# Performance work log

Hardware: AMD Instinct MI355X
Metric: run time of the kernel (lower is better)

## Reference

```python
import jax, jax.numpy as jnp
import numpy as np

DIM = 4096
NUM_HEAD = 32
NUM_KV_HEAD = 8
ROPE_THETA = 10000.0
B, T = 2, 2048


def apply_rope(x, start_pos=0, theta=ROPE_THETA):
    # x: [B, T, H, d_head]; rotate half-split pairs by position-dependent angles
    d = x.shape[-1]
    half = d // 2
    inv_freq = 1.0 / (theta ** (jnp.arange(0, half, dtype=jnp.float32) / half))
    pos = jnp.arange(x.shape[1], dtype=jnp.float32) + start_pos  # [T]
    ang = pos[:, None] * inv_freq[None, :]                       # [T, half]
    cos = jnp.cos(ang)[None, :, None, :]
    sin = jnp.sin(ang)[None, :, None, :]
    x1, x2 = x[..., :half], x[..., half:]
    return jnp.concatenate([x1 * cos - x2 * sin, x1 * sin + x2 * cos], axis=-1)


def setup_inputs() -> dict:
    key = jax.random.key(0)
    ks = jax.random.split(key, 5)
    scale = 0.02
    X = jax.random.normal(ks[0], (B, T, DIM), dtype=jnp.float32)
    Wq = jax.random.normal(ks[1], (DIM, DIM), dtype=jnp.float32) * scale
    Wk = jax.random.normal(ks[2], (DIM, DIM // NUM_HEAD * NUM_KV_HEAD), dtype=jnp.float32) * scale
    Wv = jax.random.normal(ks[3], (DIM, DIM // NUM_HEAD * NUM_KV_HEAD), dtype=jnp.float32) * scale
    Wo = jax.random.normal(ks[4], (DIM, DIM), dtype=jnp.float32) * scale
    return {"X": X, "Wq": Wq, "Wk": Wk, "Wv": Wv, "Wo": Wo}


def reference(X, Wq, Wk, Wv, Wo):
    Bs, Ts, C = X.shape
    H, Hkv = NUM_HEAD, NUM_KV_HEAD
    dh = C // H
    G = H // Hkv  # GQA group size

    Q = apply_rope((X @ Wq).reshape(Bs, Ts, H, dh))      # [B,T,H,dh]
    K = apply_rope((X @ Wk).reshape(Bs, Ts, Hkv, dh))    # [B,T,Hkv,dh]
    V = (X @ Wv).reshape(Bs, Ts, Hkv, dh)                # [B,T,Hkv,dh]

    # [B,Hkv,G,T,dh]: grouped layout equivalent to repeat_interleave on head dim
    Qh = Q.transpose(0, 2, 1, 3).reshape(Bs, Hkv, G, Ts, dh)
    Kh = K.transpose(0, 2, 1, 3)  # [B,Hkv,T,dh]
    Vh = V.transpose(0, 2, 1, 3)

    scores = jnp.einsum('bkgtd,bksd->bkgts', Qh, Kh) / jnp.sqrt(jnp.float32(dh))
    causal = jnp.tril(jnp.ones((Ts, Ts), dtype=bool))
    scores = jnp.where(causal[None, None, None], scores, -jnp.inf)
    attn = jax.nn.softmax(scores, axis=-1)
    out = jnp.einsum('bkgts,bksd->bkgtd', attn, Vh)       # [B,Hkv,G,T,dh]
    out = out.reshape(Bs, H, Ts, dh).transpose(0, 2, 1, 3).reshape(Bs, Ts, C)
    return out @ Wo
```

## Files before the change

### kernel.cpp

```cpp
#include <hip/hip_runtime.h>
#include <hip/hip_bf16.h>
#include <cstdint>
#include <cstddef>

#define B_   2
#define T_   2048
#define DIM_ 4096
#define H_   32
#define HKV_ 8
#define DH_  128
#define MROWS (B_*T_)

typedef __bf16 bf16_t;
typedef bf16_t bf16x8 __attribute__((ext_vector_type(8)));
typedef bf16_t bf16x4 __attribute__((ext_vector_type(4)));
typedef float  f32x4  __attribute__((ext_vector_type(4)));

typedef __attribute__((address_space(1))) void gvoid_t;
typedef __attribute__((address_space(3))) void lvoid_t;

__device__ __forceinline__ void gld_lds16(const void* g, void* l) {
  __builtin_amdgcn_global_load_lds((gvoid_t*)g, (lvoid_t*)l, 16, 0, 0);
}

__device__ __forceinline__ f32x4 mfma16(bf16x8 a, bf16x8 b, f32x4 c) {
  return __builtin_amdgcn_mfma_f32_16x16x32_bf16(a, b, c, 0, 0, 0);
}

__global__ void cast_f32_bf16(const float* __restrict__ in,
                              bf16_t* __restrict__ out, int n4) {
  int i = blockIdx.x * blockDim.x + threadIdx.x;
  if (i < n4) {
    float4 v = ((const float4*)in)[i];
    bf16x4 o;
    o[0] = (bf16_t)v.x; o[1] = (bf16_t)v.y; o[2] = (bf16_t)v.z; o[3] = (bf16_t)v.w;
    ((bf16x4*)out)[i] = o;
  }
}

__global__ void transpose_cast(const float* __restrict__ in,
                               bf16_t* __restrict__ out, int K, int N) {
  __shared__ float tile[32][33];
  int n0 = blockIdx.x * 32, k0 = blockIdx.y * 32;
  int tx = threadIdx.x, ty = threadIdx.y;
#pragma unroll
  for (int j = 0; j < 4; ++j)
    tile[ty + j*8][tx] = in[(size_t)(k0 + ty + j*8) * N + n0 + tx];
  __syncthreads();
#pragma unroll
  for (int j = 0; j < 4; ++j)
    out[(size_t)(n0 + ty + j*8) * K + k0 + tx] = (bf16_t)tile[tx][ty + j*8];
}

template <int OUT_F32>
__global__ __launch_bounds__(256, 2)
void gemm_bt(const bf16_t* __restrict__ A, const bf16_t* __restrict__ BT,
             void* __restrict__ C, int M, int N, int K) {
  __shared__ __align__(16) bf16_t Als[128 * 32];
  __shared__ __align__(16) bf16_t Bls[128 * 32];
  const int tid  = threadIdx.x;
  const int wave = tid >> 6, lane = tid & 63;
  const int quad = lane >> 4, l16 = lane & 15;
  const int wm = wave >> 1, wn = wave & 1;
  const int m0 = blockIdx.y * 128, n0 = blockIdx.x * 128;

  f32x4 acc[4][4] = {};

  const int srow = lane >> 2;
  const int scol = (lane & 3) * 8;

  for (int k0 = 0; k0 < K; k0 += 32) {
#pragma unroll
    for (int c = 0; c < 2; ++c) {
      int ch = wave * 2 + c;
      gld_lds16(A + (size_t)(m0 + ch*16 + srow) * K + k0 + scol,
                &Als[ch*512 + srow*32 + scol]);
    }
#pragma unroll
    for (int c = 0; c < 2; ++c) {
      int ch = wave * 2 + c;
      gld_lds16(BT + (size_t)(n0 + ch*16 + srow) * K + k0 + scol,
                &Bls[ch*512 + srow*32 + scol]);
    }
    __syncthreads();

    bf16x8 af[4], bfr[4];
#pragma unroll
    for (int mi = 0; mi < 4; ++mi)
      af[mi] = *(const bf16x8*)&Als[(wm*64 + mi*16 + l16)*32 + quad*8];
#pragma unroll
    for (int ni = 0; ni < 4; ++ni)
      bfr[ni] = *(const bf16x8*)&Bls[(wn*64 + ni*16 + l16)*32 + quad*8];
#pragma unroll
    for (int mi = 0; mi < 4; ++mi)
#pragma unroll
      for (int ni = 0; ni < 4; ++ni)
        acc[mi][ni] = mfma16(af[mi], bfr[ni], acc[mi][ni]);
    __syncthreads();
  }

#pragma unroll
  for (int mi = 0; mi < 4; ++mi)
#pragma unroll
    for (int ni = 0; ni < 4; ++ni)
#pragma unroll
      for (int r = 0; r < 4; ++r) {
        int row = m0 + wm*64 + mi*16 + quad*4 + r;
        int col = n0 + wn*64 + ni*16 + l16;
        if (OUT_F32)
          ((float*)C)[(size_t)row * N + col] = acc[mi][ni][r];
        else
          ((bf16_t*)C)[(size_t)row * N + col] = (bf16_t)acc[mi][ni][r];
      }
}

__global__ void rope_kernel(bf16_t* __restrict__ X, int Hn, int total) {
  int i = blockIdx.x * blockDim.x + threadIdx.x;
  if (i >= total) return;
  int d   = i & 63;
  int rem = i >> 6;
  int h   = rem % Hn; rem /= Hn;
  int t   = rem % T_;
  int b   = rem / T_;
  size_t base = ((size_t)(b * T_ + t) * Hn + h) * DH_;
  float x1 = (float)X[base + d];
  float x2 = (float)X[base + 64 + d];
  float inv_freq = expf(-(float)d * 0.14391156758f);
  float ang = (float)t * inv_freq;
  float s, c;
  sincosf(ang, &s, &c);
  X[base + d]      = (bf16_t)(x1 * c - x2 * s);
  X[base + 64 + d] = (bf16_t)(x1 * s + x2 * c);
}

__global__ void v_transpose(const bf16_t* __restrict__ Vb,
                            bf16_t* __restrict__ VT) {
  __shared__ bf16_t tile[32][33];
  int t0 = blockIdx.x * 32;
  int d0 = blockIdx.y * 32;
  int bk = blockIdx.z;
  int b = bk >> 3, kv = bk & 7;
  int tx = threadIdx.x, ty = threadIdx.y;
#pragma unroll
  for (int j = 0; j < 4; ++j)
    tile[ty + j*8][tx] =
        Vb[(size_t)(b * T_ + t0 + ty + j*8) * (HKV_*DH_) + kv*DH_ + d0 + tx];
  __syncthreads();
#pragma unroll
  for (int j = 0; j < 4; ++j)
    VT[((size_t)bk * DH_ + d0 + ty + j*8) * T_ + t0 + tx] = tile[tx][ty + j*8];
}

__global__ __launch_bounds__(256, 2)
void flash_attn(const bf16_t* __restrict__ Qb, const bf16_t* __restrict__ Kb,
                const bf16_t* __restrict__ VT, bf16_t* __restrict__ Ob) {
  __shared__ __align__(16) bf16_t Kls[64 * 128];
  __shared__ __align__(16) bf16_t Vls[128 * 64];
  __shared__ __align__(16) bf16_t Pls[128 * 72];

  const int tid = threadIdx.x, wave = tid >> 6, lane = tid & 63;
  const int quad = lane >> 4, l16 = lane & 15;
  const int qt = blockIdx.x, h = blockIdx.y, b = blockIdx.z;
  const int kv = h >> 2;

  bf16x8 q[2][4];
#pragma unroll
  for (int mi = 0; mi < 2; ++mi) {
    const bf16_t* base =
        Qb + (size_t)(b*T_ + qt*128 + wave*32 + mi*16 + l16) * DIM_ + h*DH_;
#pragma unroll
    for (int kk = 0; kk < 4; ++kk)
      q[mi][kk] = *(const bf16x8*)(base + kk*32 + quad*8);
  }

  float m_st[2][4], l_st[2][4];
  f32x4 o_acc[2][8] = {};
#pragma unroll
  for (int mi = 0; mi < 2; ++mi)
#pragma unroll
    for (int r = 0; r < 4; ++r) { m_st[mi][r] = -3e38f; l_st[mi][r] = 0.f; }

  const int nkv = 2 * (qt + 1);
  for (int kvt = 0; kvt < nkv; ++kvt) {
    __syncthreads();

    {
      int r_in = lane >> 4, cphys = lane & 15;
#pragma unroll
      for (int c = 0; c < 4; ++c) {
        int ch = wave * 4 + c;
        int krow = ch * 4 + r_in;
        int clog = cphys ^ (krow & 7);
        gld_lds16(Kb + (size_t)(b*T_ + kvt*64 + krow) * (HKV_*DH_) + kv*DH_ + clog*8,
                  &Kls[ch*512 + lane*8]);
      }
      int r8 = lane >> 3, c8 = lane & 7;
#pragma unroll
      for (int c = 0; c < 4; ++c) {
        int ch = wave * 4 + c;
        int drow = ch * 8 + r8;
        int clog = c8 ^ (drow & 7);
        gld_lds16(VT + ((size_t)(b*HKV_ + kv) * DH_ + drow) * T_ + kvt*64 + clog*8,
                  &Vls[ch*512 + lane*8]);
      }
    }
    __syncthreads();

    f32x4 s[2][4] = {};
#pragma unroll
    for (int kk = 0; kk < 4; ++kk) {
      bf16x8 kf[4];
#pragma unroll
      for (int ni = 0; ni < 4; ++ni) {
        int krow = ni*16 + l16;
        int cphys = (kk*4 + quad) ^ (krow & 7);
        kf[ni] = *(const bf16x8*)&Kls[krow*128 + cphys*8];
      }
#pragma unroll
      for (int mi = 0; mi < 2; ++mi)
#pragma unroll
        for (int ni = 0; ni < 4; ++ni)
          s[mi][ni] = mfma16(q[mi][kk], kf[ni], s[mi][ni]);
    }

    const float sc = 0.08838834764831845f;
    const bool need_mask = (kvt >= 2*qt);
#pragma unroll
    for (int mi = 0; mi < 2; ++mi) {
      float al[4];
#pragma unroll
      for (int r = 0; r < 4; ++r) {
        int rpos = qt*128 + wave*32 + mi*16 + quad*4 + r;
        float mx = -3e38f;
#pragma unroll
        for (int ni = 0; ni < 4; ++ni) {
          float v = s[mi][ni][r] * sc;
          if (need_mask) {
            int cpos = kvt*64 + ni*16 + l16;
            if (cpos > rpos) v = -3e38f;
          }
          s[mi][ni][r] = v;
          mx = fmaxf(mx, v);
        }
#pragma unroll
        for (int off = 1; off < 16; off <<= 1)
          mx = fmaxf(mx, __shfl_xor(mx, off, 64));
        float mnew = fmaxf(m_st[mi][r], mx);
        float alpha = __expf(m_st[mi][r] - mnew);
        m_st[mi][r] = mnew;
        float rs = 0.f;
#pragma unroll
        for (int ni = 0; ni < 4; ++ni) {
          float p = __expf(s[mi][ni][r] - mnew);
          s[mi][ni][r] = p;
          rs += p;
        }
#pragma unroll
        for (int off = 1; off < 16; off <<= 1)
          rs += __shfl_xor(rs, off, 64);
        l_st[mi][r] = l_st[mi][r] * alpha + rs;
        al[r] = alpha;
      }
#pragma unroll
      for (int ni = 0; ni < 8; ++ni)
#pragma unroll
        for (int r = 0; r < 4; ++r) o_acc[mi][ni][r] *= al[r];
#pragma unroll
      for (int ni = 0; ni < 4; ++ni)
#pragma unroll
        for (int r = 0; r < 4; ++r) {
          int prow = wave*32 + mi*16 + quad*4 + r;
          Pls[prow*72 + ni*16 + l16] = (bf16_t)s[mi][ni][r];
        }
    }
    __syncthreads();

#pragma unroll
    for (int kk = 0; kk < 2; ++kk) {
      bf16x8 pf[2], vf[8];
#pragma unroll
      for (int mi = 0; mi < 2; ++mi) {
        int prow = wave*32 + mi*16 + l16;
        pf[mi] = *(const bf16x8*)&Pls[prow*72 + kk*32 + quad*8];
      }
#pragma unroll
      for (int ni = 0; ni < 8; ++ni) {
        int drow = ni*16 + l16;
        int cphys = (kk*4 + quad) ^ (drow & 7);
        vf[ni] = *(const bf16x8*)&Vls[drow*64 + cphys*8];
      }
#pragma unroll
      for (int mi = 0; mi < 2; ++mi)
#pragma unroll
        for (int ni = 0; ni < 8; ++ni)
          o_acc[mi][ni] = mfma16(pf[mi], vf[ni], o_acc[mi][ni]);
    }
  }

#pragma unroll
  for (int mi = 0; mi < 2; ++mi) {
    float inv[4];
#pragma unroll
    for (int r = 0; r < 4; ++r) inv[r] = 1.f / l_st[mi][r];
#pragma unroll
    for (int ni = 0; ni < 8; ++ni)
#pragma unroll
      for (int r = 0; r < 4; ++r) {
        size_t row = (size_t)(b*T_ + qt*128 + wave*32 + mi*16 + quad*4 + r);
        int col = h*DH_ + ni*16 + l16;
        Ob[row * DIM_ + col] = (bf16_t)(o_acc[mi][ni][r] * inv[r]);
      }
  }
}

extern "C" void kernel_launch(void* const* d_in, const int* in_sizes, int n_in,
                              void* d_out, int out_size, void* d_ws, size_t ws_size,
                              hipStream_t stream) {
  const float* X  = (const float*)d_in[0];
  const float* Wq = (const float*)d_in[1];
  const float* Wk = (const float*)d_in[2];
  const float* Wv = (const float*)d_in[3];
  const float* Wo = (const float*)d_in[4];
  float* out = (float*)d_out;

  char* ws = (char*)d_ws;
  const size_t SZ_X  = (size_t)MROWS * DIM_ * 2;
  const size_t SZ_WQ = (size_t)DIM_ * DIM_ * 2;
  const size_t SZ_WK = (size_t)DIM_ * 1024 * 2;
  bf16_t* Xb  = (bf16_t*)(ws);
  bf16_t* WqT = (bf16_t*)(ws + SZ_X);
  bf16_t* WkT = (bf16_t*)(ws + SZ_X + SZ_WQ);
  bf16_t* WvT = (bf16_t*)(ws + SZ_X + SZ_WQ + SZ_WK);
  bf16_t* WoT = (bf16_t*)(ws + SZ_X + SZ_WQ + 2*SZ_WK);
  bf16_t* Qb  = (bf16_t*)(ws + SZ_X + 2*SZ_WQ + 2*SZ_WK);
  bf16_t* Kb  = (bf16_t*)(ws + 2*SZ_X + 2*SZ_WQ + 2*SZ_WK);
  bf16_t* Vb  = (bf16_t*)(ws + 2*SZ_X + 2*SZ_WQ + 3*SZ_WK);
  bf16_t* VT  = (bf16_t*)(ws + 2*SZ_X + 2*SZ_WQ + 4*SZ_WK);
  bf16_t* Ob  = Xb;

  {
    int n4 = MROWS * DIM_ / 4;
    cast_f32_bf16<<<(n4 + 255)/256, 256, 0, stream>>>(X, Xb, n4);
  }
  transpose_cast<<<dim3(DIM_/32, DIM_/32), dim3(32,8), 0, stream>>>(Wq, WqT, DIM_, DIM_);
  transpose_cast<<<dim3(1024/32, DIM_/32), dim3(32,8), 0, stream>>>(Wk, WkT, DIM_, 1024);
  transpose_cast<<<dim3(1024/32, DIM_/32), dim3(32,8), 0, stream>>>(Wv, WvT, DIM_, 1024);
  transpose_cast<<<dim3(DIM_/32, DIM_/32), dim3(32,8), 0, stream>>>(Wo, WoT, DIM_, DIM_);

  gemm_bt<0><<<dim3(DIM_/128, MROWS/128), 256, 0, stream>>>(Xb, WqT, Qb, MROWS, DIM_, DIM_);
  gemm_bt<0><<<dim3(1024/128, MROWS/128), 256, 0, stream>>>(Xb, WkT, Kb, MROWS, 1024, DIM_);
  gemm_bt<0><<<dim3(1024/128, MROWS/128), 256, 0, stream>>>(Xb, WvT, Vb, MROWS, 1024, DIM_);

  {
    int totq = B_ * T_ * H_ * 64;
    rope_kernel<<<(totq + 255)/256, 256, 0, stream>>>(Qb, H_, totq);
    int totk = B_ * T_ * HKV_ * 64;
    rope_kernel<<<(totk + 255)/256, 256, 0, stream>>>(Kb, HKV_, totk);
  }

  v_transpose<<<dim3(T_/32, DH_/32, B_*HKV_), dim3(32,8), 0, stream>>>(Vb, VT);

  flash_attn<<<dim3(T_/128, H_, B_), 256, 0, stream>>>(Qb, Kb, VT, Ob);

  gemm_bt<1><<<dim3(DIM_/128, MROWS/128), 256, 0, stream>>>(Ob, WoT, out, MROWS, DIM_, DIM_);
}
```

Baseline: 995.5 us.

## Double-buffer K/V tiles, reverse tile order, and defer softmax rescaling in flash attention

K and V tiles now alternate between two LDS buffers, so the next tile's global-to-LDS copy is issued while the current tile is computed. This removes one barrier per iteration, and the barrier after the P write is dropped because each wave reads only its own P rows. Query tiles run in reverse order so the longest causal blocks start first, and the softmax scale is folded into exp2 arguments. Output rescaling is skipped while the running max stays within a threshold. The P buffer switches from padding to an XOR swizzle, and s_setprio raises wave priority around the MFMA sections. These changes add complexity and LDS usage, and deferred rescaling relies on the threshold keeping exponentials in range.

```diff
diff --git a/kernel.cpp b/kernel.cpp
--- a/kernel.cpp
+++ b/kernel.cpp
@@ -154,13 +154,14 @@
 __global__ __launch_bounds__(256, 2)
 void flash_attn(const bf16_t* __restrict__ Qb, const bf16_t* __restrict__ Kb,
                 const bf16_t* __restrict__ VT, bf16_t* __restrict__ Ob) {
-  __shared__ __align__(16) bf16_t Kls[64 * 128];
-  __shared__ __align__(16) bf16_t Vls[128 * 64];
-  __shared__ __align__(16) bf16_t Pls[128 * 72];
+  __shared__ __align__(16) bf16_t Kls[2][64 * 128];
+  __shared__ __align__(16) bf16_t Vls[2][128 * 64];
+  __shared__ __align__(16) bf16_t Pls[128 * 64];
 
   const int tid = threadIdx.x, wave = tid >> 6, lane = tid & 63;
   const int quad = lane >> 4, l16 = lane & 15;
-  const int qt = blockIdx.x, h = blockIdx.y, b = blockIdx.z;
+  const int qt = (int)gridDim.x - 1 - (int)blockIdx.x;
+  const int h = blockIdx.y, b = blockIdx.z;
   const int kv = h >> 2;
 
   bf16x8 q[2][4];
@@ -178,35 +179,43 @@
 #pragma unroll
   for (int mi = 0; mi < 2; ++mi)
 #pragma unroll
-    for (int r = 0; r < 4; ++r) { m_st[mi][r] = -3e38f; l_st[mi][r] = 0.f; }
+    for (int r = 0; r < 4; ++r) { m_st[mi][r] = -1e30f; l_st[mi][r] = 0.f; }
 
   const int nkv = 2 * (qt + 1);
+
+  auto stage = [&](int kvt, int pb) {
+    int r_in = lane >> 4, cph = lane & 15;
+#pragma unroll
+    for (int c = 0; c < 4; ++c) {
+      int ch = wave * 4 + c;
+      int krow = ch * 4 + r_in;
+      int clog = cph ^ (krow & 7);
+      gld_lds16(Kb + (size_t)(b*T_ + kvt*64 + krow) * (HKV_*DH_) + kv*DH_ + clog*8,
+                &Kls[pb][ch*512 + lane*8]);
+    }
+    int r8 = lane >> 3, c8 = lane & 7;
+#pragma unroll
+    for (int c = 0; c < 4; ++c) {
+      int ch = wave * 4 + c;
+      int drow = ch * 8 + r8;
+      int clog = c8 ^ (drow & 7);
+      gld_lds16(VT + ((size_t)(b*HKV_ + kv) * DH_ + drow) * T_ + kvt*64 + clog*8,
+                &Vls[pb][ch*512 + lane*8]);
+    }
+  };
+
+  stage(0, 0);
+
+  const float S2 = 0.08838834764831845f * 1.4426950408889634f;
+  const float THRraw = 8.0f / 0.08838834764831845f;
+
   for (int kvt = 0; kvt < nkv; ++kvt) {
+    const int p = kvt & 1;
     __syncthreads();
-
-    {
-      int r_in = lane >> 4, cphys = lane & 15;
-#pragma unroll
-      for (int c = 0; c < 4; ++c) {
-        int ch = wave * 4 + c;
-        int krow = ch * 4 + r_in;
-        int clog = cphys ^ (krow & 7);
-        gld_lds16(Kb + (size_t)(b*T_ + kvt*64 + krow) * (HKV_*DH_) + kv*DH_ + clog*8,
-                  &Kls[ch*512 + lane*8]);
-      }
-      int r8 = lane >> 3, c8 = lane & 7;
-#pragma unroll
-      for (int c = 0; c < 4; ++c) {
-        int ch = wave * 4 + c;
-        int drow = ch * 8 + r8;
-        int clog = c8 ^ (drow & 7);
-        gld_lds16(VT + ((size_t)(b*HKV_ + kv) * DH_ + drow) * T_ + kvt*64 + clog*8,
-                  &Vls[ch*512 + lane*8]);
-      }
-    }
-    __syncthreads();
+    if (kvt + 1 < nkv) stage(kvt + 1, p ^ 1);
 
     f32x4 s[2][4] = {};
+    __builtin_amdgcn_s_setprio(1);
 #pragma unroll
     for (int kk = 0; kk < 4; ++kk) {
       bf16x8 kf[4];
@@ -214,7 +223,7 @@
       for (int ni = 0; ni < 4; ++ni) {
         int krow = ni*16 + l16;
         int cphys = (kk*4 + quad) ^ (krow & 7);
-        kf[ni] = *(const bf16x8*)&Kls[krow*128 + cphys*8];
+        kf[ni] = *(const bf16x8*)&Kls[p][krow*128 + cphys*8];
       }
 #pragma unroll
       for (int mi = 0; mi < 2; ++mi)
@@ -222,72 +231,101 @@
         for (int ni = 0; ni < 4; ++ni)
           s[mi][ni] = mfma16(q[mi][kk], kf[ni], s[mi][ni]);
     }
-
-    const float sc = 0.08838834764831845f;
+    __builtin_amdgcn_s_setprio(0);
+
     const bool need_mask = (kvt >= 2*qt);
 #pragma unroll
     for (int mi = 0; mi < 2; ++mi) {
-      float al[4];
+      float mx[4];
 #pragma unroll
       for (int r = 0; r < 4; ++r) {
         int rpos = qt*128 + wave*32 + mi*16 + quad*4 + r;
-        float mx = -3e38f;
+        float m = -1e30f;
 #pragma unroll
         for (int ni = 0; ni < 4; ++ni) {
-          float v = s[mi][ni][r] * sc;
+          float v = s[mi][ni][r];
           if (need_mask) {
             int cpos = kvt*64 + ni*16 + l16;
-            if (cpos > rpos) v = -3e38f;
+            if (cpos > rpos) v = -1e30f;
           }
           s[mi][ni][r] = v;
-          mx = fmaxf(mx, v);
+          m = fmaxf(m, v);
         }
 #pragma unroll
         for (int off = 1; off < 16; off <<= 1)
-          mx = fmaxf(mx, __shfl_xor(mx, off, 64));
-        float mnew = fmaxf(m_st[mi][r], mx);
-        float alpha = __expf(m_st[mi][r] - mnew);
-        m_st[mi][r] = mnew;
-        float rs = 0.f;
-#pragma unroll
-        for (int ni = 0; ni < 4; ++ni) {
-          float p = __expf(s[mi][ni][r] - mnew);
-          s[mi][ni][r] = p;
-          rs += p;
+          m = fmaxf(m, __shfl_xor(m, off, 64));
+        mx[r] = m;
+      }
+      bool defer = true;
+#pragma unroll
+      for (int r = 0; r < 4; ++r)
+        defer = defer && (mx[r] <= m_st[mi][r] + THRraw);
+      if (__all(defer)) {
+#pragma unroll
+        for (int r = 0; r < 4; ++r) {
+          float mn2 = m_st[mi][r] * S2;
+          float rs = 0.f;
+#pragma unroll
+          for (int ni = 0; ni < 4; ++ni) {
+            float pv = __builtin_amdgcn_exp2f(fmaf(s[mi][ni][r], S2, -mn2));
+            s[mi][ni][r] = pv;
+            rs += pv;
+          }
+#pragma unroll
+          for (int off = 1; off < 16; off <<= 1)
+            rs += __shfl_xor(rs, off, 64);
+          l_st[mi][r] += rs;
         }
-#pragma unroll
-        for (int off = 1; off < 16; off <<= 1)
-          rs += __shfl_xor(rs, off, 64);
-        l_st[mi][r] = l_st[mi][r] * alpha + rs;
-        al[r] = alpha;
-      }
-#pragma unroll
-      for (int ni = 0; ni < 8; ++ni)
-#pragma unroll
-        for (int r = 0; r < 4; ++r) o_acc[mi][ni][r] *= al[r];
+      } else {
+        float al[4];
+#pragma unroll
+        for (int r = 0; r < 4; ++r) {
+          float mnew = fmaxf(m_st[mi][r], mx[r]);
+          al[r] = __builtin_amdgcn_exp2f((m_st[mi][r] - mnew) * S2);
+          m_st[mi][r] = mnew;
+          float mn2 = mnew * S2;
+          float rs = 0.f;
+#pragma unroll
+          for (int ni = 0; ni < 4; ++ni) {
+            float pv = __builtin_amdgcn_exp2f(fmaf(s[mi][ni][r], S2, -mn2));
+            s[mi][ni][r] = pv;
+            rs += pv;
+          }
+#pragma unroll
+          for (int off = 1; off < 16; off <<= 1)
+            rs += __shfl_xor(rs, off, 64);
+          l_st[mi][r] = l_st[mi][r] * al[r] + rs;
+        }
+#pragma unroll
+        for (int ni = 0; ni < 8; ++ni)
+#pragma unroll
+          for (int r = 0; r < 4; ++r) o_acc[mi][ni][r] *= al[r];
+      }
 #pragma unroll
       for (int ni = 0; ni < 4; ++ni)
 #pragma unroll
         for (int r = 0; r < 4; ++r) {
           int prow = wave*32 + mi*16 + quad*4 + r;
-          Pls[prow*72 + ni*16 + l16] = (bf16_t)s[mi][ni][r];
+          int g = (ni*2 + (l16 >> 3)) ^ (prow & 7);
+          Pls[prow*64 + g*8 + (l16 & 7)] = (bf16_t)s[mi][ni][r];
         }
     }
-    __syncthreads();
-
+
+    __builtin_amdgcn_s_setprio(1);
 #pragma unroll
     for (int kk = 0; kk < 2; ++kk) {
       bf16x8 pf[2], vf[8];
 #pragma unroll
       for (int mi = 0; mi < 2; ++mi) {
         int prow = wave*32 + mi*16 + l16;
-        pf[mi] = *(const bf16x8*)&Pls[prow*72 + kk*32 + quad*8];
+        int g = (kk*4 + quad) ^ (prow & 7);
+        pf[mi] = *(const bf16x8*)&Pls[prow*64 + g*8];
       }
 #pragma unroll
       for (int ni = 0; ni < 8; ++ni) {
         int drow = ni*16 + l16;
         int cphys = (kk*4 + quad) ^ (drow & 7);
-        vf[ni] = *(const bf16x8*)&Vls[drow*64 + cphys*8];
+        vf[ni] = *(const bf16x8*)&Vls[p][drow*64 + cphys*8];
       }
 #pragma unroll
       for (int mi = 0; mi < 2; ++mi)
@@ -295,6 +333,7 @@
         for (int ni = 0; ni < 8; ++ni)
           o_acc[mi][ni] = mfma16(pf[mi], vf[ni], o_acc[mi][ni]);
     }
+    __builtin_amdgcn_s_setprio(0);
   }
 
 #pragma unroll
```

Measured after the change: 1.075 ms. 7.9% more time.
